# Optimization experiments

Measured on AMD Instinct MI355X. Metric: run time of the kernel, lower is better.

The kernel has to match this reference:

```python
import jax, jax.numpy as jnp
import numpy as np

VOCAB = 50000
DIM = 50
B = 131072
CTX = 10
NEG = 10
EPS = 1e-10


def setup_inputs() -> dict:
    key = jax.random.key(0)
    k1, k2, k3, k4, k5 = jax.random.split(key, 5)
    return {
        "context_idxs": jax.random.randint(k1, (B, CTX), 0, VOCAB),
        "pos_target": jax.random.randint(k2, (B,), 0, VOCAB),
        "neg_samples": jax.random.randint(k3, (B, NEG), 0, VOCAB),
        "in_embed_W": jax.random.normal(k4, (VOCAB, DIM), dtype=jnp.float32),
        "out_embed_W": jax.random.normal(k5, (VOCAB, DIM), dtype=jnp.float32),
    }


def reference(context_idxs, pos_target, neg_samples, in_embed_W, out_embed_W):
    # context_vec: [B, D] = mean over context window of in_embed gathers
    context_vec = in_embed_W[context_idxs].mean(axis=1)
    # positive score: [B]
    pos_embeds = out_embed_W[pos_target]                      # [B, D]
    pos_score = jnp.sum(context_vec * pos_embeds, axis=1)     # [B]
    pos_loss = jnp.log(jax.nn.sigmoid(pos_score) + EPS)       # [B]
    # negative scores: [B, K] = bmm(neg_embeds [B,K,D], context_vec [B,D,1])
    neg_embeds = out_embed_W[neg_samples]                     # [B, K, D]
    neg_score = jnp.einsum("bkd,bd->bk", neg_embeds, context_vec)
    neg_loss = jnp.log(jax.nn.sigmoid(-neg_score) + EPS).sum(axis=1)  # [B]
    return -(pos_loss + neg_loss).mean()
```

## Files before the change

kernel.cpp:

```cpp
#include <hip/hip_runtime.h>
#include <hip/hip_fp8.h>

#define VOCAB 50000
#define DIM   50
#define B_TOT 131072
#define CTX   10
#define NEG   10
#define EPS_F 1e-10f
#define PAIRS (B_TOT / 2)

constexpr int TPB    = 256;
constexpr int BLOCKS = 4096;
constexpr int NWAVES = BLOCKS * (TPB / 64);
constexpr int ITERS  = PAIRS / NWAVES;
static_assert(PAIRS % NWAVES == 0, "exact division required");

constexpr size_t ROW8_B  = 64;
constexpr size_t TAB8_B  = (size_t)VOCAB * ROW8_B;
constexpr size_t WS_NEED = 2 * TAB8_B + BLOCKS * 4;

constexpr int BUF_W = 48 * 16;

typedef float vf2 __attribute__((ext_vector_type(2)));

static __device__ __forceinline__ void fp8x8_to_f32x8(unsigned long long w,
                                                      float* f) {
#if __has_builtin(__builtin_amdgcn_cvt_pk_f32_fp8)
    const int lo = (int)(unsigned int)w;
    const int hi = (int)(unsigned int)(w >> 32);
    vf2 a = __builtin_amdgcn_cvt_pk_f32_fp8(lo, false);
    vf2 b = __builtin_amdgcn_cvt_pk_f32_fp8(lo, true);
    vf2 c = __builtin_amdgcn_cvt_pk_f32_fp8(hi, false);
    vf2 d = __builtin_amdgcn_cvt_pk_f32_fp8(hi, true);
    f[0] = a[0]; f[1] = a[1]; f[2] = b[0]; f[3] = b[1];
    f[4] = c[0]; f[5] = c[1]; f[6] = d[0]; f[7] = d[1];
#else
    #pragma unroll
    for (int i = 0; i < 8; ++i) {
        __hip_fp8_e4m3 v;
        v.__x = (unsigned char)(w >> (8 * i));
        f[i] = (float)v;
    }
#endif
}

template <int CTRL>
static __device__ __forceinline__ float dpp_add(float x) {
    const int y = __builtin_amdgcn_mov_dpp(__float_as_int(x), CTRL, 0xF, 0xF, true);
    return x + __int_as_float(y);
}

__global__ __launch_bounds__(256) void cbow_convert(
    const float* __restrict__ inW, const float* __restrict__ outW,
    unsigned short* __restrict__ ws8)
{
    const int t = blockIdx.x * 256 + threadIdx.x;
    const int per_tab = VOCAB * 32;
    if (t >= 2 * per_tab) return;
    const int tab = t / per_tab;
    const int rem = t - tab * per_tab;
    const int r   = rem >> 5;
    const int j   = rem & 31;

    unsigned short u = 0;
    if (j < 25) {
        const float2* src2 = (const float2*)(tab ? outW : inW);
        const float2  v    = src2[r * 25 + j];
#if __has_builtin(__builtin_amdgcn_cvt_pk_fp8_f32)
        const int pk = __builtin_amdgcn_cvt_pk_fp8_f32(v.x, v.y, 0, false);
        u = (unsigned short)(pk & 0xffff);
#else
        __hip_fp8_e4m3 a(v.x), b(v.y);
        u = (unsigned short)(a.__x | (b.__x << 8));
#endif
    }
    ws8[(size_t)tab * (VOCAB * 32) + (size_t)r * 32 + j] = u;
}

__global__ __launch_bounds__(TPB, 8) void cbow_loss_fp8(
    const int* __restrict__ ctx_idx,
    const int* __restrict__ pos_idx,
    const int* __restrict__ neg_idx,
    const unsigned short* __restrict__ ws8,
    float* __restrict__ partials)
{
    __shared__ unsigned int lds[(TPB / 64) * BUF_W];

    const int lane = threadIdx.x & 63;
    const int sub  = lane >> 5;
    const int l    = lane & 31;
    const int quad = lane >> 2;
    const int qb   = (lane & 3) * 16;
    const int g    = (l >> 3) & 3;
    const int j    = l & 7;

    const int wave  = threadIdx.x >> 6;
    unsigned int* wbase = lds + wave * BUF_W;
    const int gwave = blockIdx.x * (TPB / 64) + wave;

    const char* in8  = (const char*)ws8;
    const char* out8 = (const char*)(ws8 + (size_t)VOCAB * 32);

    auto idx_addr = [&](int b) -> const int* {
        if (l < CTX)           return ctx_idx + b * CTX + l;
        if (l == CTX)          return pos_idx + b;
        if (l < CTX + 1 + NEG) return neg_idx + b * NEG + (l - CTX - 1);
        return pos_idx + b;
    };

    float loss_lane = 0.f;

    int my_idx = *idx_addr(2 * gwave + sub);

    #pragma unroll
    for (int i = 0; i < ITERS; ++i) {
        #pragma unroll
        for (int t = 0; t < 3; ++t) {
            const int row  = t * 16 + quad;
            const int crow = (row > 41) ? 41 : row;
            const int sample = (crow >= 21) ? 1 : 0;
            const int slot   = crow - 21 * sample;
            const int idx = __shfl(my_idx, sample * 32 + slot);
            if (t < 2 || lane < 40) {
                const char* tb = (slot < CTX) ? in8 : out8;
                const char* ga = tb + ((size_t)(unsigned)idx << 6) + qb;
                __builtin_amdgcn_global_load_lds(
                    (const __attribute__((address_space(1))) unsigned int*)ga,
                    (__attribute__((address_space(3))) unsigned int*)(wbase + t * 256),
                    16, 0, 0);
            }
        }

        const int np = (i + 1 < ITERS) ? gwave + (i + 1) * NWAVES : gwave;
        const int next_idx = *idx_addr(2 * np + sub);

        asm volatile("s_waitcnt vmcnt(0)" ::: "memory");

        const char* smp = (const char*)wbase + sub * (21 * 64);

        float cv[8] = {0.f, 0.f, 0.f, 0.f, 0.f, 0.f, 0.f, 0.f};
        #pragma unroll
        for (int s = 0; s < 5; ++s) {
            const int r = (g & 1) * 5 + s;
            const unsigned long long w =
                *(const unsigned long long*)(smp + r * 64 + j * 8);
            float f[8];
            fp8x8_to_f32x8(w, f);
            #pragma unroll
            for (int d = 0; d < 8; ++d) cv[d] += f[d];
        }
        #pragma unroll
        for (int d = 0; d < 8; ++d) cv[d] = dpp_add<0x128>(cv[d]);

        #pragma unroll
        for (int p = 0; p < 3; ++p) {
            int r = 10 + 4 * p + g;
            r = (r > 20) ? 20 : r;
            const unsigned long long w =
                *(const unsigned long long*)(smp + r * 64 + j * 8);
            float f[8];
            fp8x8_to_f32x8(w, f);
            float prod = 0.f;
            #pragma unroll
            for (int d = 0; d < 8; ++d) prod = fmaf(cv[d], f[d], prod);
            prod = dpp_add<0xB1>(prod);
            prod = dpp_add<0x4E>(prod);
            prod = dpp_add<0x141>(prod);

            const bool valid = (j == 0) && !(p == 2 && g == 3);
            const float sc   = prod * (1.f / CTX);
            const float z    = (p == 0 && g == 0) ? sc : -sc;
            const float sig  = 1.f / (1.f + __expf(-z));
            const float c    = __logf(sig + EPS_F);
            loss_lane += valid ? c : 0.f;
        }

        my_idx = next_idx;
    }

    loss_lane += __shfl_xor(loss_lane, 1);
    loss_lane += __shfl_xor(loss_lane, 2);
    loss_lane += __shfl_xor(loss_lane, 4);
    loss_lane += __shfl_xor(loss_lane, 8);
    loss_lane += __shfl_xor(loss_lane, 16);
    loss_lane += __shfl_xor(loss_lane, 32);

    __shared__ float s_part[TPB / 64];
    if (lane == 0) s_part[wave] = loss_lane;
    __syncthreads();
    if (threadIdx.x == 0) {
        float s = 0.f;
        #pragma unroll
        for (int w = 0; w < TPB / 64; ++w) s += s_part[w];
        partials[blockIdx.x] = s;
    }
}

__global__ __launch_bounds__(TPB) void cbow_loss_f32(
    const int*   __restrict__ ctx_idx, const int* __restrict__ pos_idx,
    const int*   __restrict__ neg_idx, const float* __restrict__ inW,
    const float* __restrict__ outW,    float* __restrict__ partials)
{
    const int lane = threadIdx.x & 63;
    const int sub  = lane >> 5;
    const int l    = lane & 31;
    const int p    = (l < 25) ? l : 24;
    const bool act = (l < 25);
    const int wave   = threadIdx.x >> 6;
    const int gwave  = blockIdx.x * (TPB / 64) + wave;
    const float2* inW2  = (const float2*)inW;
    const float2* outW2 = (const float2*)outW;

    float loss_lane = 0.f;
    for (int pair = gwave; pair < PAIRS; pair += NWAVES) {
        const int b = 2 * pair + sub;
        float cvx = 0.f, cvy = 0.f;
        #pragma unroll
        for (int jj = 0; jj < CTX; ++jj) {
            const float2 v = inW2[ctx_idx[b * CTX + jj] * 25 + p];
            cvx += v.x; cvy += v.y;
        }
        cvx *= (1.f / CTX); cvy *= (1.f / CTX);
        float packed = 0.f;
        #pragma unroll
        for (int r = 0; r <= NEG; ++r) {
            const int idx = (r == 0) ? pos_idx[b] : neg_idx[b * NEG + r - 1];
            const float2 v = outW2[idx * 25 + p];
            float prod = act ? (cvx * v.x + cvy * v.y) : 0.f;
            prod += __shfl_xor(prod, 1);
            prod += __shfl_xor(prod, 2);
            prod += __shfl_xor(prod, 4);
            prod += __shfl_xor(prod, 8);
            prod += __shfl_xor(prod, 16);
            packed = (l == r) ? prod : packed;
        }
        const float z   = (l == 0) ? packed : -packed;
        const float sig = 1.f / (1.f + __expf(-z));
        loss_lane += (l < NEG + 1) ? __logf(sig + EPS_F) : 0.f;
    }
    loss_lane += __shfl_xor(loss_lane, 1);
    loss_lane += __shfl_xor(loss_lane, 2);
    loss_lane += __shfl_xor(loss_lane, 4);
    loss_lane += __shfl_xor(loss_lane, 8);
    loss_lane += __shfl_xor(loss_lane, 16);
    loss_lane += __shfl_xor(loss_lane, 32);
    __shared__ float s_part[TPB / 64];
    if (lane == 0) s_part[wave] = loss_lane;
    __syncthreads();
    if (threadIdx.x == 0) {
        float s = 0.f;
        #pragma unroll
        for (int w = 0; w < TPB / 64; ++w) s += s_part[w];
        partials[blockIdx.x] = s;
    }
}

__global__ __launch_bounds__(256) void cbow_finalize(
    const float* __restrict__ partials, float* __restrict__ out)
{
    float s = 0.f;
    for (int i = threadIdx.x; i < BLOCKS; i += 256) s += partials[i];
    #pragma unroll
    for (int k = 32; k >= 1; k >>= 1) s += __shfl_xor(s, k);
    __shared__ float sm[4];
    const int w = threadIdx.x >> 6;
    if ((threadIdx.x & 63) == 0) sm[w] = s;
    __syncthreads();
    if (threadIdx.x == 0)
        out[0] = -(sm[0] + sm[1] + sm[2] + sm[3]) * (1.f / (float)B_TOT);
}

extern "C" void kernel_launch(void* const* d_in, const int* in_sizes, int n_in,
                              void* d_out, int out_size, void* d_ws, size_t ws_size,
                              hipStream_t stream) {
    const int*   ctx_idx = (const int*)  d_in[0];
    const int*   pos_idx = (const int*)  d_in[1];
    const int*   neg_idx = (const int*)  d_in[2];
    const float* inW     = (const float*)d_in[3];
    const float* outW    = (const float*)d_in[4];
    float*       out     = (float*)d_out;

    if (ws_size >= WS_NEED) {
        unsigned short* ws8 = (unsigned short*)d_ws;
        float* partials = (float*)((char*)d_ws + 2 * TAB8_B);
        const int conv_threads = 2 * VOCAB * 32;
        cbow_convert<<<(conv_threads + 255) / 256, 256, 0, stream>>>(inW, outW, ws8);
        cbow_loss_fp8<<<BLOCKS, TPB, 0, stream>>>(ctx_idx, pos_idx, neg_idx, ws8, partials);
        cbow_finalize<<<1, 256, 0, stream>>>(partials, out);
    } else {
        float* partials = (float*)d_ws;
        cbow_loss_f32<<<BLOCKS, TPB, 0, stream>>>(ctx_idx, pos_idx, neg_idx, inW, outW, partials);
        cbow_finalize<<<1, 256, 0, stream>>>(partials, out);
    }
}
```

Baseline: 121.5 us.

## Use packed vf2 math, simplify log-sigmoid, and double block count

Doubles the grid from 4096 to 8192 blocks, halving the loop iterations per wave. The fp8 conversion and dot products now use 2-wide float vectors so the compiler can emit packed FP32 add and multiply instructions. log(sigmoid(z)+eps) is replaced by -log(1+exp(-z)), which drops a division and the epsilon term. This changes results slightly when sigmoid is near zero, and the larger grid adds per-block launch and reduction overhead.

New measurement: 114.4 us. 5.8% less time.

```diff
diff --git a/kernel.cpp b/kernel.cpp
--- a/kernel.cpp
+++ b/kernel.cpp
@@ -10,7 +10,7 @@
 #define PAIRS (B_TOT / 2)
 
 constexpr int TPB    = 256;
-constexpr int BLOCKS = 4096;
+constexpr int BLOCKS = 8192;
 constexpr int NWAVES = BLOCKS * (TPB / 64);
 constexpr int ITERS  = PAIRS / NWAVES;
 static_assert(PAIRS % NWAVES == 0, "exact division required");
@@ -23,23 +23,23 @@
 
 typedef float vf2 __attribute__((ext_vector_type(2)));
 
-static __device__ __forceinline__ void fp8x8_to_f32x8(unsigned long long w,
-                                                      float* f) {
+static __device__ __forceinline__ void fp8x8_to_vf2x4(unsigned long long w,
+                                                      vf2* f) {
 #if __has_builtin(__builtin_amdgcn_cvt_pk_f32_fp8)
     const int lo = (int)(unsigned int)w;
     const int hi = (int)(unsigned int)(w >> 32);
-    vf2 a = __builtin_amdgcn_cvt_pk_f32_fp8(lo, false);
-    vf2 b = __builtin_amdgcn_cvt_pk_f32_fp8(lo, true);
-    vf2 c = __builtin_amdgcn_cvt_pk_f32_fp8(hi, false);
-    vf2 d = __builtin_amdgcn_cvt_pk_f32_fp8(hi, true);
-    f[0] = a[0]; f[1] = a[1]; f[2] = b[0]; f[3] = b[1];
-    f[4] = c[0]; f[5] = c[1]; f[6] = d[0]; f[7] = d[1];
+    f[0] = __builtin_amdgcn_cvt_pk_f32_fp8(lo, false);
+    f[1] = __builtin_amdgcn_cvt_pk_f32_fp8(lo, true);
+    f[2] = __builtin_amdgcn_cvt_pk_f32_fp8(hi, false);
+    f[3] = __builtin_amdgcn_cvt_pk_f32_fp8(hi, true);
 #else
     #pragma unroll
-    for (int i = 0; i < 8; ++i) {
-        __hip_fp8_e4m3 v;
-        v.__x = (unsigned char)(w >> (8 * i));
-        f[i] = (float)v;
+    for (int i = 0; i < 4; ++i) {
+        __hip_fp8_e4m3 a, b;
+        a.__x = (unsigned char)(w >> (16 * i));
+        b.__x = (unsigned char)(w >> (16 * i + 8));
+        f[i][0] = (float)a;
+        f[i][1] = (float)b;
     }
 #endif
 }
@@ -138,19 +138,22 @@
 
         const char* smp = (const char*)wbase + sub * (21 * 64);
 
-        float cv[8] = {0.f, 0.f, 0.f, 0.f, 0.f, 0.f, 0.f, 0.f};
+        vf2 cv[4] = {vf2{0.f, 0.f}, vf2{0.f, 0.f}, vf2{0.f, 0.f}, vf2{0.f, 0.f}};
         #pragma unroll
         for (int s = 0; s < 5; ++s) {
             const int r = (g & 1) * 5 + s;
             const unsigned long long w =
                 *(const unsigned long long*)(smp + r * 64 + j * 8);
-            float f[8];
-            fp8x8_to_f32x8(w, f);
+            vf2 f[4];
+            fp8x8_to_vf2x4(w, f);
             #pragma unroll
-            for (int d = 0; d < 8; ++d) cv[d] += f[d];
-        }
-        #pragma unroll
-        for (int d = 0; d < 8; ++d) cv[d] = dpp_add<0x128>(cv[d]);
+            for (int d = 0; d < 4; ++d) cv[d] += f[d];
+        }
+        #pragma unroll
+        for (int d = 0; d < 4; ++d) {
+            cv[d][0] = dpp_add<0x128>(cv[d][0]);
+            cv[d][1] = dpp_add<0x128>(cv[d][1]);
+        }
 
         #pragma unroll
         for (int p = 0; p < 3; ++p) {
@@ -158,11 +161,12 @@
             r = (r > 20) ? 20 : r;
             const unsigned long long w =
                 *(const unsigned long long*)(smp + r * 64 + j * 8);
-            float f[8];
-            fp8x8_to_f32x8(w, f);
-            float prod = 0.f;
+            vf2 f[4];
+            fp8x8_to_vf2x4(w, f);
+            vf2 acc2 = {0.f, 0.f};
             #pragma unroll
-            for (int d = 0; d < 8; ++d) prod = fmaf(cv[d], f[d], prod);
+            for (int d = 0; d < 4; ++d) acc2 += cv[d] * f[d];
+            float prod = acc2[0] + acc2[1];
             prod = dpp_add<0xB1>(prod);
             prod = dpp_add<0x4E>(prod);
             prod = dpp_add<0x141>(prod);
@@ -170,8 +174,7 @@
             const bool valid = (j == 0) && !(p == 2 && g == 3);
             const float sc   = prod * (1.f / CTX);
             const float z    = (p == 0 && g == 0) ? sc : -sc;
-            const float sig  = 1.f / (1.f + __expf(-z));
-            const float c    = __logf(sig + EPS_F);
+            const float c    = -__logf(1.f + __expf(-z));
             loss_lane += valid ? c : 0.f;
         }
 
```
